# Performance work log

Hardware: AMD Instinct MI355X
Metric: run time of the kernel (lower is better)

## Reference

```python
import jax, jax.numpy as jnp
import numpy as np

T, B, I, H = 512, 32, 512, 512  # seq_len, batch, input_size, hidden_size


def setup_inputs() -> dict:
    key = jax.random.key(0)
    ks = jax.random.split(key, 6)
    s = 0.05  # small weight scale keeps tanh/sigmoid in non-saturated range
    return {
        "x": jax.random.normal(ks[0], (T, B, I), jnp.float32),
        "h0": jax.random.normal(ks[1], (2, B, H), jnp.float32),
        "w_ih": jax.random.normal(ks[2], (2, 3 * H, I), jnp.float32) * s,  # gate-major [r,z,n]
        "w_hh": jax.random.normal(ks[3], (2, 3 * H, H), jnp.float32) * s,
        "b_ih": jax.random.normal(ks[4], (2, 3 * H), jnp.float32) * s,
        "b_hh": jax.random.normal(ks[5], (2, 3 * H), jnp.float32) * s,
    }


def _gru_scan(xg, h0, whh, bhh):
    """One-direction GRU. xg: (T,B,3H) = x @ Wih^T + b_ih precomputed."""
    def step(h, xg_t):
        gh = h @ whh.T + bhh                     # (B,3H) recurrent gates
        ir, iz, inn = jnp.split(xg_t, 3, axis=-1)
        hr, hz, hn = jnp.split(gh, 3, axis=-1)
        r = jax.nn.sigmoid(ir + hr)
        z = jax.nn.sigmoid(iz + hz)
        n = jnp.tanh(inn + r * hn)               # PyTorch GRU: r gates (Whh_n h + b_hh_n)
        h_new = (1.0 - z) * n + z * h
        return h_new, h_new
    hT, ys = jax.lax.scan(step, h0, xg)
    return hT, ys


def reference(x, h0, w_ih, w_hh, b_ih, b_hh):
    # Input projections for all timesteps at once (one big GEMM per direction).
    xg_f = jnp.einsum('tbi,gi->tbg', x, w_ih[0]) + b_ih[0]
    xg_b = jnp.einsum('tbi,gi->tbg', x, w_ih[1]) + b_ih[1]
    hT_f, y_f = _gru_scan(xg_f, h0[0], w_hh[0], b_hh[0])
    hT_b, y_b_rev = _gru_scan(xg_b[::-1], h0[1], w_hh[1], b_hh[1])
    y_b = y_b_rev[::-1]                          # align reverse outputs to original time
    y = jnp.concatenate([y_f, y_b], axis=-1)     # (T,B,2H)
    hn = jnp.stack([hT_f, hT_b])                 # (2,B,H)
    return y, hn
```

## Files before the change

### kernel.cpp

```cpp
#include <hip/hip_runtime.h>


constexpr int T_ = 512, B_ = 32, I_ = 512, H_ = 512;
constexpr int NBLK = 256;
constexpr int NTHR = 512;
constexpr int ROW_F4 = 128;
constexpr int FLAG_STRIDE = 16;

typedef float f32x4 __attribute__((ext_vector_type(4)));

__device__ __forceinline__ float sigmoid_(float v) {
    return 1.0f / (1.0f + __expf(-v));
}
__device__ __forceinline__ float tanh_(float v) {
    v = fminf(fmaxf(v, -15.0f), 15.0f);
    float e = __expf(2.0f * v);
    return (e - 1.0f) / (e + 1.0f);
}

__global__ __launch_bounds__(NTHR, 1) void gru_bidir(
    const float* __restrict__ x, const float* __restrict__ h0,
    const float* __restrict__ w_ih, const float* __restrict__ w_hh,
    const float* __restrict__ b_ih, const float* __restrict__ b_hh,
    float* __restrict__ out, unsigned* __restrict__ flags)
{
    extern __shared__ float lds[];
    float4* lds4 = (float4*)lds;
    float*  ldsh = lds + 24 * 512;

    const int bid = blockIdx.x;
    const int d   = bid >> 7;
    const int s   = bid & 127;
    const int tid = threadIdx.x;

    for (int idx = tid; idx < 24 * ROW_F4; idx += NTHR) {
        const int row = idx >> 7;
        const int f4p = idx & 127;
        const int m   = row >> 2, jjr = row & 3;
        const int g   = (m < 3) ? m : m - 3;
        const float* W = (m < 3) ? w_ih : w_hh;
        const float4* src =
            (const float4*)(W + ((size_t)d * (3 * H_) + g * H_ + s * 4 + jjr) * (size_t)I_);
        lds4[row * ROW_F4 + f4p] = src[f4p];
    }
    __syncthreads();

    const int q     = tid & 15;
    const int bglow = (tid >> 4) & 3;
    const int upper = tid >> 6;
    const int jj    = upper & 3;
    const int bgh   = upper >> 2;
    const int b0    = bgh * 16 + bglow * 4;
    const int j     = s * 4 + jj;

    const float bihr = b_ih[d * 1536 + j];
    const float bihz = b_ih[d * 1536 + 512 + j];
    const float bihn = b_ih[d * 1536 + 1024 + j];
    const float bhhr = b_hh[d * 1536 + j];
    const float bhhz = b_hh[d * 1536 + 512 + j];
    const float bhhn = b_hh[d * 1536 + 1024 + j];

    const float4* wri = lds4 + (0 * 4 + jj) * ROW_F4 + q;
    const float4* wzi = lds4 + (1 * 4 + jj) * ROW_F4 + q;
    const float4* wni = lds4 + (2 * 4 + jj) * ROW_F4 + q;
    const float4* wrh = lds4 + (3 * 4 + jj) * ROW_F4 + q;
    const float4* wzh = lds4 + (4 * 4 + jj) * ROW_F4 + q;
    const float4* wnh = lds4 + (5 * 4 + jj) * ROW_F4 + q;

    unsigned* flagdir = flags + d * 128 * FLAG_STRIDE;

    float xar[4], xaz[4], xan[4];
    auto xpart = [&](int t) {
#pragma unroll
        for (int bi = 0; bi < 4; ++bi) { xar[bi] = 0.f; xaz[bi] = 0.f; xan[bi] = 0.f; }
        const float4* xr[4];
#pragma unroll
        for (int bi = 0; bi < 4; ++bi)
            xr[bi] = (const float4*)(x + ((size_t)t * B_ + (b0 + bi)) * I_) + q;
#pragma unroll 2
        for (int i = 0; i < 8; ++i) {
            const int o = i * 16;
            const float4 w0 = wri[o], w1 = wzi[o], w2 = wni[o];
#pragma unroll
            for (int bi = 0; bi < 4; ++bi) {
                const float4 xv = xr[bi][o];
                xar[bi] = fmaf(w0.x, xv.x, fmaf(w0.y, xv.y, fmaf(w0.z, xv.z, fmaf(w0.w, xv.w, xar[bi]))));
                xaz[bi] = fmaf(w1.x, xv.x, fmaf(w1.y, xv.y, fmaf(w1.z, xv.z, fmaf(w1.w, xv.w, xaz[bi]))));
                xan[bi] = fmaf(w2.x, xv.x, fmaf(w2.y, xv.y, fmaf(w2.z, xv.z, fmaf(w2.w, xv.w, xan[bi]))));
            }
        }
    };

    xpart(d ? T_ - 1 : 0);

    for (int k = 0; k < T_; ++k) {
        const int t = d ? (T_ - 1 - k) : k;

        if (k > 0 && tid < 64) {
            const unsigned tgt = (unsigned)k;
            unsigned* f0 = flagdir + tid * FLAG_STRIDE;
            unsigned* f1 = flagdir + (64 + tid) * FLAG_STRIDE;
            for (;;) {
                const unsigned a = __hip_atomic_load(f0, __ATOMIC_RELAXED, __HIP_MEMORY_SCOPE_AGENT);
                const unsigned b = __hip_atomic_load(f1, __ATOMIC_RELAXED, __HIP_MEMORY_SCOPE_AGENT);
                if (__all(a >= tgt && b >= tgt)) break;
                __builtin_amdgcn_s_sleep(1);
            }
        }
        __syncthreads();

        const float* hbase;
        int hstride, hoff;
        if (k == 0) {
            hbase = h0 + (size_t)d * B_ * H_; hstride = H_; hoff = 0;
        } else {
            const int tp = d ? (t + 1) : (t - 1);
            hbase = out + (size_t)tp * B_ * (2 * H_); hstride = 2 * H_; hoff = d * H_;
        }

        float hp[4];
#pragma unroll
        for (int bi = 0; bi < 4; ++bi)
            hp[bi] = hbase[(size_t)(b0 + bi) * hstride + hoff + j];

        float ahr[4], ahz[4], ahn[4];
#pragma unroll
        for (int bi = 0; bi < 4; ++bi) { ahr[bi] = 0.f; ahz[bi] = 0.f; ahn[bi] = 0.f; }
        const float4* hr[4];
#pragma unroll
        for (int bi = 0; bi < 4; ++bi)
            hr[bi] = (const float4*)(hbase + (size_t)(b0 + bi) * hstride + hoff) + q;
#pragma unroll 2
        for (int i = 0; i < 8; ++i) {
            const int o = i * 16;
            const float4 w3 = wrh[o], w4 = wzh[o], w5 = wnh[o];
#pragma unroll
            for (int bi = 0; bi < 4; ++bi) {
                const float4 hv = hr[bi][o];
                ahr[bi] = fmaf(w3.x, hv.x, fmaf(w3.y, hv.y, fmaf(w3.z, hv.z, fmaf(w3.w, hv.w, ahr[bi]))));
                ahz[bi] = fmaf(w4.x, hv.x, fmaf(w4.y, hv.y, fmaf(w4.z, hv.z, fmaf(w4.w, hv.w, ahz[bi]))));
                ahn[bi] = fmaf(w5.x, hv.x, fmaf(w5.y, hv.y, fmaf(w5.z, hv.z, fmaf(w5.w, hv.w, ahn[bi]))));
            }
        }

#pragma unroll
        for (int bi = 0; bi < 4; ++bi) {
            float ar = xar[bi] + ahr[bi];
            float az = xaz[bi] + ahz[bi];
            float an = xan[bi];
            float ah = ahn[bi];
#pragma unroll
            for (int m = 1; m < 16; m <<= 1) {
                ar += __shfl_xor(ar, m);
                az += __shfl_xor(az, m);
                an += __shfl_xor(an, m);
                ah += __shfl_xor(ah, m);
            }
            const float r = sigmoid_(ar + bihr + bhhr);
            const float z = sigmoid_(az + bihz + bhhz);
            const float n = tanh_(an + bihn + r * (ah + bhhn));
            const float hnew = (1.0f - z) * n + z * hp[bi];
            if (q == 0) ldsh[(b0 + bi) * 4 + jj] = hnew;
        }
        __syncthreads();

        if (tid < 64) {
            if (tid < 32) {
                const f32x4 hv4 = *(const f32x4*)&ldsh[tid * 4];
                float* dst = out + ((size_t)t * B_ + tid) * (2 * H_) + d * H_ + s * 4;
                asm volatile("global_store_dwordx4 %0, %1, off sc0 sc1"
                             :: "v"(dst), "v"(hv4) : "memory");
                if (k == T_ - 1) {
                    float* hn = out + (size_t)T_ * B_ * (2 * H_)
                              + ((size_t)d * B_ + tid) * H_ + s * 4;
                    *(f32x4*)hn = hv4;
                }
            }
            asm volatile("s_waitcnt vmcnt(0)" ::: "memory");
            if (tid == 0)
                __hip_atomic_store(flagdir + s * FLAG_STRIDE, (unsigned)(k + 1),
                                   __ATOMIC_RELAXED, __HIP_MEMORY_SCOPE_AGENT);
        }

        if (k + 1 < T_) xpart(d ? (T_ - 2 - k) : (k + 1));
    }
}

extern "C" void kernel_launch(void* const* d_in, const int* in_sizes, int n_in,
                              void* d_out, int out_size, void* d_ws, size_t ws_size,
                              hipStream_t stream) {
    const float* x    = (const float*)d_in[0];
    const float* h0   = (const float*)d_in[1];
    const float* w_ih = (const float*)d_in[2];
    const float* w_hh = (const float*)d_in[3];
    const float* b_ih = (const float*)d_in[4];
    const float* b_hh = (const float*)d_in[5];
    float* out = (float*)d_out;
    unsigned* flags = (unsigned*)d_ws;

    (void)hipMemsetAsync(d_ws, 0, 2 * 128 * FLAG_STRIDE * sizeof(unsigned), stream);

    void* args[] = { (void*)&x, (void*)&h0, (void*)&w_ih, (void*)&w_hh,
                     (void*)&b_ih, (void*)&b_hh, (void*)&out, (void*)&flags };
    const unsigned shmem = (24 * 512 + 128) * sizeof(float);
    (void)hipLaunchCooperativeKernel((void*)gru_bidir, dim3(NBLK), dim3(NTHR),
                                     args, shmem, stream);
}
```

Baseline: 3.848 ms.

## Split GRU recurrence across 512 blocks with two hidden units each

Launches a new persistent cooperative kernel with 512 blocks, each owning 2 hidden units instead of 4. This halves per-block weight storage and per-thread FMA work per step, so the whole grid spreads across more CUs. The cost is that each block now polls 256 flags per direction instead of 128, which adds synchronisation traffic. The old kernel is kept as a fallback in case the cooperative launch fails.

```diff
diff --git a/kernel.cpp b/kernel.cpp
--- a/kernel.cpp
+++ b/kernel.cpp
@@ -2,12 +2,12 @@
 
 
 constexpr int T_ = 512, B_ = 32, I_ = 512, H_ = 512;
-constexpr int NBLK = 256;
 constexpr int NTHR = 512;
 constexpr int ROW_F4 = 128;
 constexpr int FLAG_STRIDE = 16;
 
 typedef float f32x4 __attribute__((ext_vector_type(4)));
+typedef float f32x2 __attribute__((ext_vector_type(2)));
 
 __device__ __forceinline__ float sigmoid_(float v) {
     return 1.0f / (1.0f + __expf(-v));
@@ -18,7 +18,172 @@
     return (e - 1.0f) / (e + 1.0f);
 }
 
-__global__ __launch_bounds__(NTHR, 1) void gru_bidir(
+__global__ __launch_bounds__(NTHR, 4) void gru_main(
+    const float* __restrict__ x, const float* __restrict__ h0,
+    const float* __restrict__ w_ih, const float* __restrict__ w_hh,
+    const float* __restrict__ b_ih, const float* __restrict__ b_hh,
+    float* __restrict__ out, unsigned* __restrict__ flags)
+{
+    extern __shared__ float lds[];
+    float4* lds4 = (float4*)lds;
+    float*  ldsh = lds + 12 * 512;
+
+    const int bid = blockIdx.x;
+    const int d   = bid >> 8;
+    const int s2  = bid & 255;
+    const int tid = threadIdx.x;
+
+    for (int idx = tid; idx < 12 * ROW_F4; idx += NTHR) {
+        const int row = idx >> 7;
+        const int f4p = idx & 127;
+        const int m   = row >> 1, jjr = row & 1;
+        const int g   = (m < 3) ? m : m - 3;
+        const float* W = (m < 3) ? w_ih : w_hh;
+        const float4* src =
+            (const float4*)(W + ((size_t)d * (3 * H_) + g * H_ + s2 * 2 + jjr) * (size_t)I_);
+        lds4[row * ROW_F4 + f4p] = src[f4p];
+    }
+    __syncthreads();
+
+    const int q  = tid & 15;
+    const int bs = (tid >> 4) & 15;
+    const int jj = tid >> 8;
+    const int b0 = bs * 2;
+    const int j  = s2 * 2 + jj;
+
+    const float bihr = b_ih[d * 1536 + j];
+    const float bihz = b_ih[d * 1536 + 512 + j];
+    const float bihn = b_ih[d * 1536 + 1024 + j];
+    const float bhhr = b_hh[d * 1536 + j];
+    const float bhhz = b_hh[d * 1536 + 512 + j];
+    const float bhhn = b_hh[d * 1536 + 1024 + j];
+
+    const float4* wri = lds4 + (0 * 2 + jj) * ROW_F4 + q;
+    const float4* wzi = lds4 + (2 + jj) * ROW_F4 + q;
+    const float4* wni = lds4 + (4 + jj) * ROW_F4 + q;
+    const float4* wrh = lds4 + (6 + jj) * ROW_F4 + q;
+    const float4* wzh = lds4 + (8 + jj) * ROW_F4 + q;
+    const float4* wnh = lds4 + (10 + jj) * ROW_F4 + q;
+
+    unsigned* flagchain = flags + (size_t)d * 256 * FLAG_STRIDE;
+
+    float xar[2], xaz[2], xan[2];
+    auto xpart = [&](int t) {
+#pragma unroll
+        for (int bi = 0; bi < 2; ++bi) { xar[bi] = 0.f; xaz[bi] = 0.f; xan[bi] = 0.f; }
+        const float4* xr0 = (const float4*)(x + ((size_t)t * B_ + b0) * I_) + q;
+        const float4* xr1 = (const float4*)(x + ((size_t)t * B_ + b0 + 1) * I_) + q;
+#pragma unroll
+        for (int i = 0; i < 8; ++i) {
+            const int o = i * 16;
+            const float4 w0 = wri[o], w1 = wzi[o], w2 = wni[o];
+            const float4 xv0 = xr0[o], xv1 = xr1[o];
+            xar[0] = fmaf(w0.x, xv0.x, fmaf(w0.y, xv0.y, fmaf(w0.z, xv0.z, fmaf(w0.w, xv0.w, xar[0]))));
+            xaz[0] = fmaf(w1.x, xv0.x, fmaf(w1.y, xv0.y, fmaf(w1.z, xv0.z, fmaf(w1.w, xv0.w, xaz[0]))));
+            xan[0] = fmaf(w2.x, xv0.x, fmaf(w2.y, xv0.y, fmaf(w2.z, xv0.z, fmaf(w2.w, xv0.w, xan[0]))));
+            xar[1] = fmaf(w0.x, xv1.x, fmaf(w0.y, xv1.y, fmaf(w0.z, xv1.z, fmaf(w0.w, xv1.w, xar[1]))));
+            xaz[1] = fmaf(w1.x, xv1.x, fmaf(w1.y, xv1.y, fmaf(w1.z, xv1.z, fmaf(w1.w, xv1.w, xaz[1]))));
+            xan[1] = fmaf(w2.x, xv1.x, fmaf(w2.y, xv1.y, fmaf(w2.z, xv1.z, fmaf(w2.w, xv1.w, xan[1]))));
+        }
+    };
+
+    xpart(d ? T_ - 1 : 0);
+
+    for (int k = 0; k < T_; ++k) {
+        const int t = d ? (T_ - 1 - k) : k;
+
+        if (k > 0 && tid < 64) {
+            const unsigned tgt = (unsigned)k;
+            unsigned* f0 = flagchain + tid * FLAG_STRIDE;
+            unsigned* f1 = f0 + 64 * FLAG_STRIDE;
+            unsigned* f2 = f0 + 128 * FLAG_STRIDE;
+            unsigned* f3 = f0 + 192 * FLAG_STRIDE;
+            for (;;) {
+                const unsigned a = __hip_atomic_load(f0, __ATOMIC_RELAXED, __HIP_MEMORY_SCOPE_AGENT);
+                const unsigned b = __hip_atomic_load(f1, __ATOMIC_RELAXED, __HIP_MEMORY_SCOPE_AGENT);
+                const unsigned c = __hip_atomic_load(f2, __ATOMIC_RELAXED, __HIP_MEMORY_SCOPE_AGENT);
+                const unsigned e = __hip_atomic_load(f3, __ATOMIC_RELAXED, __HIP_MEMORY_SCOPE_AGENT);
+                if (__all(a >= tgt && b >= tgt && c >= tgt && e >= tgt)) break;
+                __builtin_amdgcn_s_sleep(1);
+            }
+        }
+        __syncthreads();
+
+        const float* hbase;
+        int hstride, hoff;
+        if (k == 0) {
+            hbase = h0 + (size_t)d * B_ * H_; hstride = H_; hoff = 0;
+        } else {
+            const int tp = d ? (t + 1) : (t - 1);
+            hbase = out + (size_t)tp * B_ * (2 * H_); hstride = 2 * H_; hoff = d * H_;
+        }
+
+        float hp0 = hbase[(size_t)b0 * hstride + hoff + j];
+        float hp1 = hbase[(size_t)(b0 + 1) * hstride + hoff + j];
+
+        float ahr[2], ahz[2], ahn[2];
+#pragma unroll
+        for (int bi = 0; bi < 2; ++bi) { ahr[bi] = 0.f; ahz[bi] = 0.f; ahn[bi] = 0.f; }
+        const float4* hr0 = (const float4*)(hbase + (size_t)b0 * hstride + hoff) + q;
+        const float4* hr1 = (const float4*)(hbase + (size_t)(b0 + 1) * hstride + hoff) + q;
+#pragma unroll
+        for (int i = 0; i < 8; ++i) {
+            const int o = i * 16;
+            const float4 w3 = wrh[o], w4 = wzh[o], w5 = wnh[o];
+            const float4 hv0 = hr0[o], hv1 = hr1[o];
+            ahr[0] = fmaf(w3.x, hv0.x, fmaf(w3.y, hv0.y, fmaf(w3.z, hv0.z, fmaf(w3.w, hv0.w, ahr[0]))));
+            ahz[0] = fmaf(w4.x, hv0.x, fmaf(w4.y, hv0.y, fmaf(w4.z, hv0.z, fmaf(w4.w, hv0.w, ahz[0]))));
+            ahn[0] = fmaf(w5.x, hv0.x, fmaf(w5.y, hv0.y, fmaf(w5.z, hv0.z, fmaf(w5.w, hv0.w, ahn[0]))));
+            ahr[1] = fmaf(w3.x, hv1.x, fmaf(w3.y, hv1.y, fmaf(w3.z, hv1.z, fmaf(w3.w, hv1.w, ahr[1]))));
+            ahz[1] = fmaf(w4.x, hv1.x, fmaf(w4.y, hv1.y, fmaf(w4.z, hv1.z, fmaf(w4.w, hv1.w, ahz[1]))));
+            ahn[1] = fmaf(w5.x, hv1.x, fmaf(w5.y, hv1.y, fmaf(w5.z, hv1.z, fmaf(w5.w, hv1.w, ahn[1]))));
+        }
+
+#pragma unroll
+        for (int bi = 0; bi < 2; ++bi) {
+            float ar = xar[bi] + ahr[bi];
+            float az = xaz[bi] + ahz[bi];
+            float an = xan[bi];
+            float ah = ahn[bi];
+#pragma unroll
+            for (int m = 1; m < 16; m <<= 1) {
+                ar += __shfl_xor(ar, m);
+                az += __shfl_xor(az, m);
+                an += __shfl_xor(an, m);
+                ah += __shfl_xor(ah, m);
+            }
+            const float hp = bi ? hp1 : hp0;
+            const float r = sigmoid_(ar + bihr + bhhr);
+            const float z = sigmoid_(az + bihz + bhhz);
+            const float n = tanh_(an + bihn + r * (ah + bhhn));
+            const float hnew = (1.0f - z) * n + z * hp;
+            if (q == 0) ldsh[(b0 + bi) * 2 + jj] = hnew;
+        }
+        __syncthreads();
+
+        if (tid < 64) {
+            if (tid < 32) {
+                const f32x2 hv2 = *(const f32x2*)&ldsh[tid * 2];
+                float* dst = out + ((size_t)t * B_ + tid) * (2 * H_) + d * H_ + s2 * 2;
+                asm volatile("global_store_dwordx2 %0, %1, off sc0 sc1"
+                             :: "v"(dst), "v"(hv2) : "memory");
+                if (k == T_ - 1) {
+                    float* hn = out + (size_t)T_ * B_ * (2 * H_)
+                              + ((size_t)d * B_ + tid) * H_ + s2 * 2;
+                    *(f32x2*)hn = hv2;
+                }
+            }
+            asm volatile("s_waitcnt vmcnt(0)" ::: "memory");
+            if (tid == 0)
+                __hip_atomic_store(flagchain + s2 * FLAG_STRIDE, (unsigned)(k + 1),
+                                   __ATOMIC_RELAXED, __HIP_MEMORY_SCOPE_AGENT);
+        }
+
+        if (k + 1 < T_) xpart(d ? (T_ - 2 - k) : (k + 1));
+    }
+}
+
+__global__ __launch_bounds__(NTHR, 1) void gru_fb(
     const float* __restrict__ x, const float* __restrict__ h0,
     const float* __restrict__ w_ih, const float* __restrict__ w_hh,
     const float* __restrict__ b_ih, const float* __restrict__ b_hh,
@@ -198,11 +363,17 @@
     float* out = (float*)d_out;
     unsigned* flags = (unsigned*)d_ws;
 
-    (void)hipMemsetAsync(d_ws, 0, 2 * 128 * FLAG_STRIDE * sizeof(unsigned), stream);
+    (void)hipMemsetAsync(d_ws, 0, 2 * 256 * FLAG_STRIDE * sizeof(unsigned), stream);
 
     void* args[] = { (void*)&x, (void*)&h0, (void*)&w_ih, (void*)&w_hh,
                      (void*)&b_ih, (void*)&b_hh, (void*)&out, (void*)&flags };
-    const unsigned shmem = (24 * 512 + 128) * sizeof(float);
-    (void)hipLaunchCooperativeKernel((void*)gru_bidir, dim3(NBLK), dim3(NTHR),
-                                     args, shmem, stream);
-}
+
+    const unsigned shmem_main = (12 * 512 + 64) * sizeof(float);
+    hipError_t err = hipLaunchCooperativeKernel((void*)gru_main, dim3(512), dim3(NTHR),
+                                                args, shmem_main, stream);
+    if (err != hipSuccess) {
+        const unsigned shmem_fb = (24 * 512 + 128) * sizeof(float);
+        (void)hipLaunchCooperativeKernel((void*)gru_fb, dim3(256), dim3(NTHR),
+                                         args, shmem_fb, stream);
+    }
+}
```

After: 10.83 ms. 2.81x slower.
